# Kernel tuning notes

Measured on AMD Instinct MI355X. Metric: run time of the kernel, lower is better.

The kernel has to match this reference:

```python
import jax, jax.numpy as jnp
import numpy as np
from math import sqrt

KEY_DIM = 128
VALUE_DIM = 128
SUMMARY_DIM = 128
QUESTION_NUM = 10000
CONCEPT_NUM = 64
B = 128
S = 128


def setup_inputs() -> dict:
    key = jax.random.key(0)
    ks = jax.random.split(key, 24)
    stdev = 1.0 / sqrt(CONCEPT_NUM + KEY_DIM)

    def lin_w(k, out_f, in_f):
        bound = 1.0 / sqrt(in_f)
        return jax.random.uniform(k, (out_f, in_f), jnp.float32, -bound, bound)

    def lin_b(k, out_f, in_f):
        bound = 1.0 / sqrt(in_f)
        return jax.random.uniform(k, (out_f,), jnp.float32, -bound, bound)

    q_emb = jax.random.normal(ks[0], (QUESTION_NUM + 1, KEY_DIM), jnp.float32)
    q_emb = q_emb.at[0].set(0.0)  # padding_idx = 0
    i_emb = jax.random.normal(ks[1], (2 * QUESTION_NUM + 1, VALUE_DIM), jnp.float32)
    i_emb = i_emb.at[0].set(0.0)

    inp = {
        "right_input": jax.random.randint(ks[2], (B, S), 0, 2 * QUESTION_NUM + 1),
        "wrong_input": jax.random.randint(ks[3], (B, S), 0, 2 * QUESTION_NUM + 1),
        "target_id": jax.random.randint(ks[4], (B,), 0, QUESTION_NUM + 1),
        "q_emb": q_emb,
        "i_emb": i_emb,
        "key_W": lin_w(ks[5], CONCEPT_NUM, KEY_DIM),  # no bias
        "erase_W": lin_w(ks[6], VALUE_DIM, VALUE_DIM),
        "erase_b": lin_b(ks[7], VALUE_DIM, VALUE_DIM),
        "add_W": lin_w(ks[8], VALUE_DIM, VALUE_DIM),
        "add_b": lin_b(ks[9], VALUE_DIM, VALUE_DIM),
        "rsum_W": lin_w(ks[10], SUMMARY_DIM, VALUE_DIM + KEY_DIM),
        "rsum_b": lin_b(ks[11], SUMMARY_DIM, VALUE_DIM + KEY_DIM),
        "wsum_W": lin_w(ks[12], SUMMARY_DIM, VALUE_DIM + KEY_DIM),
        "wsum_b": lin_b(ks[13], SUMMARY_DIM, VALUE_DIM + KEY_DIM),
        "succ_W": lin_w(ks[14], 1, SUMMARY_DIM),
        "succ_b": lin_b(ks[15], 1, SUMMARY_DIM),
        "fail_W": lin_w(ks[16], 1, SUMMARY_DIM),
        "fail_b": lin_b(ks[17], 1, SUMMARY_DIM),
        "diff_W": lin_w(ks[18], 1, KEY_DIM),
        "diff_b": lin_b(ks[19], 1, KEY_DIM),
        "right_mem_init": jax.random.uniform(ks[20], (VALUE_DIM, CONCEPT_NUM), jnp.float32, -stdev, stdev),
        "wrong_mem_init": jax.random.uniform(ks[21], (VALUE_DIM, CONCEPT_NUM), jnp.float32, -stdev, stdev),
    }
    return inp


def reference(right_input, wrong_input, target_id, q_emb, i_emb, key_W,
              erase_W, erase_b, add_W, add_b, rsum_W, rsum_b, wsum_W, wsum_b,
              succ_W, succ_b, fail_W, fail_b, diff_W, diff_b,
              right_mem_init, wrong_mem_init):
    Q = (i_emb.shape[0] - 1) // 2
    batch = right_input.shape[0]

    def corr(qid):  # (B,) -> (B, C) correlation weights
        return jax.nn.softmax(q_emb[qid] @ key_W.T, axis=-1)

    def update(mem, inter):
        # mem: (B, V, C); inter: (B,) interaction ids
        vec = i_emb[inter]                                  # (B, V)
        e = jax.nn.sigmoid(vec @ erase_W.T + erase_b)       # (B, V)
        a = jnp.tanh(vec @ add_W.T + add_b)                 # (B, V)
        qid = inter - Q * (inter > Q).astype(inter.dtype)
        w = corr(qid)                                       # (B, C)
        # erase/add are outer products w (x) e, w (x) a -> (B, V, C)
        return mem * (1.0 - e[:, :, None] * w[:, None, :]) + a[:, :, None] * w[:, None, :]

    def step(carry, xs):
        rm, wm = carry
        ri, wi = xs
        return (update(rm, ri), update(wm, wi)), None

    rm0 = jnp.broadcast_to(right_mem_init, (batch,) + right_mem_init.shape)
    wm0 = jnp.broadcast_to(wrong_mem_init, (batch,) + wrong_mem_init.shape)
    (rm, wm), _ = jax.lax.scan(step, (rm0, wm0), (right_input.T, wrong_input.T))

    qv = q_emb[target_id]                                   # (B, K)
    w_t = corr(target_id)                                   # (B, C)
    right_read = jnp.einsum('bvc,bc->bv', rm, w_t)          # (B, V)
    wrong_read = jnp.einsum('bvc,bc->bv', wm, w_t)

    r_sum = jnp.tanh(jnp.concatenate([right_read, qv], axis=-1) @ rsum_W.T + rsum_b)
    w_sum = jnp.tanh(jnp.concatenate([wrong_read, qv], axis=-1) @ wsum_W.T + wsum_b)

    success_level = jnp.tanh(r_sum @ succ_W.T + succ_b)     # (B, 1)
    failure_level = jnp.tanh(w_sum @ fail_W.T + fail_b)     # (B, 1)
    difficulty_level = jnp.tanh(qv @ diff_W.T + diff_b)     # (B, 1)

    success_count = jnp.sum(jnp.clip(right_input, 0, 1)).astype(jnp.float32)
    failure_count = jnp.sum(jnp.clip(wrong_input, 0, 1)).astype(jnp.float32)

    out = (success_level * jax.nn.sigmoid(success_count)
           + failure_level * jax.nn.sigmoid(failure_count)
           - difficulty_level * 2.0)
    return out
```

## Files before the change

### kernel.cpp

```cpp
#include <hip/hip_runtime.h>
#include <hip/hip_bf16.h>

#define BB 128
#define SS 128
#define VD 128
#define CN 64
#define KD 128
#define QN 10000

typedef __attribute__((ext_vector_type(8))) short bf16x8;
typedef __attribute__((ext_vector_type(4))) float f32x4;

__device__ __forceinline__ float bflo(unsigned int u) { return __uint_as_float(u << 16); }
__device__ __forceinline__ float bfhi(unsigned int u) { return __uint_as_float(u & 0xffff0000u); }
__device__ __forceinline__ unsigned int cvtpk(float lo, float hi) {
    __hip_bfloat162 h2 = __float22bfloat162_rn(make_float2(lo, hi));
    unsigned int r; __builtin_memcpy(&r, &h2, 4); return r;
}
__device__ __forceinline__ float fast_tanh(float x) {
    float e = __expf(2.0f * x);
    return 1.0f - 2.0f / (e + 1.0f);
}
__device__ __forceinline__ float fast_sig(float x) {
    return 1.0f / (1.0f + __expf(-x));
}

__global__ __launch_bounds__(256) void k_wcnt(
    const float* __restrict__ erase_W, const float* __restrict__ add_W,
    const float* __restrict__ key_W, unsigned short* __restrict__ Bfrag,
    const int* __restrict__ ri, const int* __restrict__ wi, float* __restrict__ sig)
{
    const int t = threadIdx.x;
    if (blockIdx.x < 20) {
        const int bid = blockIdx.x * 4 + (t >> 6);
        const int l = t & 63;
        const int n = (bid >> 2) * 16 + (l & 15);
        const int k0 = (bid & 3) * 32 + (l >> 4) * 8;
        const float* src;
        if (n < 128)      src = erase_W + (size_t)n * KD + k0;
        else if (n < 256) src = add_W + (size_t)(n - 128) * KD + k0;
        else              src = key_W + (size_t)(n - 256) * KD + k0;
        float4 fa = ((const float4*)src)[0];
        float4 fb = ((const float4*)src)[1];
        uint4 o = make_uint4(cvtpk(fa.x, fa.y), cvtpk(fa.z, fa.w), cvtpk(fb.x, fb.y), cvtpk(fb.z, fb.w));
        *(uint4*)(Bfrag + ((size_t)bid * 64 + l) * 8) = o;
    } else {
        __shared__ int sr_s[4], sw_s[4];
        const int4* r4 = (const int4*)ri;
        const int4* w4 = (const int4*)wi;
        int sr = 0, sw = 0;
        #pragma unroll 4
        for (int p = 0; p < 16; ++p) {
            int4 a = r4[p * 256 + t];
            int4 b = w4[p * 256 + t];
            sr += (a.x >= 1) + (a.y >= 1) + (a.z >= 1) + (a.w >= 1);
            sw += (b.x >= 1) + (b.y >= 1) + (b.z >= 1) + (b.w >= 1);
        }
        for (int off = 1; off < 64; off <<= 1) { sr += __shfl_xor(sr, off); sw += __shfl_xor(sw, off); }
        int wid = t >> 6;
        if ((t & 63) == 0) { sr_s[wid] = sr; sw_s[wid] = sw; }
        __syncthreads();
        if (t == 0) {
            int SR = sr_s[0]+sr_s[1]+sr_s[2]+sr_s[3];
            int SW = sw_s[0]+sw_s[1]+sw_s[2]+sw_s[3];
            sig[0] = 1.0f / (1.0f + __expf(-(float)SR));
            sig[1] = 1.0f / (1.0f + __expf(-(float)SW));
        }
    }
}

__global__ __launch_bounds__(1024, 4) void k_chain(
    const int* __restrict__ ri, const int* __restrict__ wi, const int* __restrict__ tgt,
    const float* __restrict__ q_emb, const float* __restrict__ i_emb,
    const float* __restrict__ key_W,
    const float* __restrict__ erase_b, const float* __restrict__ add_b,
    const unsigned short* __restrict__ Bfrag,
    const float* __restrict__ rmem0, const float* __restrict__ wmem0,
    float* __restrict__ readbuf)
{
    __shared__ __align__(16) unsigned int lds_ea[SS * VD];
    __shared__ __align__(16) char xab[32 * 1024];
    __shared__ __align__(16) float logits[SS * 68];
    __shared__ __align__(16) unsigned short lds_w[SS * CN];
    __shared__ float q_t[KD];
    __shared__ float logit_t[CN];
    __shared__ float wt_lds[CN];
    __shared__ int qid_s[SS], ir_s[SS];
    __shared__ float psum[8 * 64];

    const int t = threadIdx.x;
    const int lane = t & 63;
    const int w = t >> 6;
    const int chain = blockIdx.x;
    const int m = chain >> 7;
    const int b = chain & 127;

    if (t < SS) {
        int inter = (m == 0 ? ri : wi)[b * SS + t];
        ir_s[t] = inter;
        qid_s[t] = (inter > QN) ? inter - QN : inter;
        q_t[t] = q_emb[(size_t)tgt[b] * KD + t];
    }
    __syncthreads();

    {
        const int r = t >> 3, o = t & 7;
        const float* src = q_emb + (size_t)qid_s[r] * KD + o * 16;
        float4 f0 = ((const float4*)src)[0];
        float4 f1 = ((const float4*)src)[1];
        float4 f2 = ((const float4*)src)[2];
        float4 f3 = ((const float4*)src)[3];
        const int bb = r * 256 + o * 32;
        const int sw = (r & 7) << 4;
        *(uint4*)(xab + (bb ^ sw))        = make_uint4(cvtpk(f0.x,f0.y), cvtpk(f0.z,f0.w), cvtpk(f1.x,f1.y), cvtpk(f1.z,f1.w));
        *(uint4*)(xab + ((bb + 16) ^ sw)) = make_uint4(cvtpk(f2.x,f2.y), cvtpk(f2.z,f2.w), cvtpk(f3.x,f3.y), cvtpk(f3.z,f3.w));
        if (t < 512) {
            const int c = t >> 3, oct = t & 7;
            const float* kw = key_W + (size_t)c * KD + oct * 16;
            float s = 0.f;
            #pragma unroll
            for (int i = 0; i < 16; ++i) s = fmaf(kw[i], q_t[oct * 16 + i], s);
            s += __shfl_xor(s, 1); s += __shfl_xor(s, 2); s += __shfl_xor(s, 4);
            if (oct == 0) logit_t[c] = s;
        }
    }
    __syncthreads();

    const int rowl = lane & 15;
    const int kb16 = (lane >> 4) * 16;
    const int rb4 = (lane >> 4) * 4;
    const int rt = w & 7;

    {
        if (w == 0) {
            float x = logit_t[lane];
            float mx = x;
            #pragma unroll
            for (int off = 1; off < 64; off <<= 1) mx = fmaxf(mx, __shfl_xor(mx, off));
            float e = __expf(x - mx);
            float ssum = e;
            #pragma unroll
            for (int off = 1; off < 64; off <<= 1) ssum += __shfl_xor(ssum, off);
            wt_lds[lane] = e / ssum;
        }
        bf16x8 afQ[4];
        const int row = rt * 16 + rowl;
        #pragma unroll
        for (int kt = 0; kt < 4; ++kt)
            afQ[kt] = *(const bf16x8*)(xab + ((row * 256 + kt * 64 + kb16) ^ ((row & 7) << 4)));
        const int nt0 = (w >> 3) * 2;
        #pragma unroll
        for (int ni = 0; ni < 2; ++ni) {
            const int nt = nt0 + ni;
            f32x4 acc = {0.f,0.f,0.f,0.f};
            #pragma unroll
            for (int kt = 0; kt < 4; ++kt) {
                bf16x8 bf = *(const bf16x8*)(Bfrag + ((size_t)((16 + nt) * 4 + kt) * 64 + lane) * 8);
                acc = __builtin_amdgcn_mfma_f32_16x16x32_bf16(afQ[kt], bf, acc, 0, 0, 0);
            }
            #pragma unroll
            for (int rr = 0; rr < 4; ++rr)
                logits[(rt * 16 + rb4 + rr) * 68 + nt * 16 + rowl] = acc[rr];
        }
    }
    __syncthreads();

    {
        const int rr = t >> 3, q = t & 7;
        const float* L = logits + rr * 68 + q * 8;
        float4 va = ((const float4*)L)[0];
        float4 vb = ((const float4*)L)[1];
        float mx = fmaxf(fmaxf(fmaxf(va.x, va.y), fmaxf(va.z, va.w)),
                         fmaxf(fmaxf(vb.x, vb.y), fmaxf(vb.z, vb.w)));
        mx = fmaxf(mx, __shfl_xor(mx, 1));
        mx = fmaxf(mx, __shfl_xor(mx, 2));
        mx = fmaxf(mx, __shfl_xor(mx, 4));
        float e0 = __expf(va.x - mx), e1 = __expf(va.y - mx), e2 = __expf(va.z - mx), e3 = __expf(va.w - mx);
        float e4 = __expf(vb.x - mx), e5 = __expf(vb.y - mx), e6 = __expf(vb.z - mx), e7 = __expf(vb.w - mx);
        float s = e0 + e1 + e2 + e3 + e4 + e5 + e6 + e7;
        s += __shfl_xor(s, 1); s += __shfl_xor(s, 2); s += __shfl_xor(s, 4);
        float inv = 1.0f / s;
        uint4 o = make_uint4(cvtpk(e0*inv, e1*inv), cvtpk(e2*inv, e3*inv),
                             cvtpk(e4*inv, e5*inv), cvtpk(e6*inv, e7*inv));
        *(uint4*)(lds_w + rr * CN + q * 8) = o;

        const float* src = i_emb + (size_t)ir_s[rr] * KD + q * 16;
        float4 f0 = ((const float4*)src)[0];
        float4 f1 = ((const float4*)src)[1];
        float4 f2 = ((const float4*)src)[2];
        float4 f3 = ((const float4*)src)[3];
        const int bb = rr * 256 + q * 32;
        const int sw = (rr & 7) << 4;
        *(uint4*)(xab + (bb ^ sw))        = make_uint4(cvtpk(f0.x,f0.y), cvtpk(f0.z,f0.w), cvtpk(f1.x,f1.y), cvtpk(f1.z,f1.w));
        *(uint4*)(xab + ((bb + 16) ^ sw)) = make_uint4(cvtpk(f2.x,f2.y), cvtpk(f2.z,f2.w), cvtpk(f3.x,f3.y), cvtpk(f3.z,f3.w));
    }
    __syncthreads();

    {
        bf16x8 afI[4];
        const int row = rt * 16 + rowl;
        #pragma unroll
        for (int kt = 0; kt < 4; ++kt)
            afI[kt] = *(const bf16x8*)(xab + ((row * 256 + kt * 64 + kb16) ^ ((row & 7) << 4)));
        const int ci0 = (w >> 3) * 4;
        #pragma unroll
        for (int ii = 0; ii < 4; ++ii) {
            const int ci = ci0 + ii;
            f32x4 ae = {0.f,0.f,0.f,0.f}, aa = {0.f,0.f,0.f,0.f};
            #pragma unroll
            for (int kt = 0; kt < 4; ++kt) {
                bf16x8 be = *(const bf16x8*)(Bfrag + ((size_t)(ci * 4 + kt) * 64 + lane) * 8);
                bf16x8 ba = *(const bf16x8*)(Bfrag + ((size_t)((8 + ci) * 4 + kt) * 64 + lane) * 8);
                ae = __builtin_amdgcn_mfma_f32_16x16x32_bf16(afI[kt], be, ae, 0, 0, 0);
                aa = __builtin_amdgcn_mfma_f32_16x16x32_bf16(afI[kt], ba, aa, 0, 0, 0);
            }
            const int cc = ci * 16 + rowl;
            const float bvE = erase_b[cc];
            const float bvA = add_b[cc];
            #pragma unroll
            for (int rr = 0; rr < 4; ++rr) {
                float e = fast_sig(ae[rr] + bvE);
                float a = fast_tanh(aa[rr] + bvA);
                lds_ea[(rt * 16 + rb4 + rr) * VD + cc] = cvtpk(e, a);
            }
        }
    }

    const int w2 = w & 7;
    const int vhalf = w2 & 1;
    const int cq = w2 >> 1;
    const int vg = lane >> 2;
    const int cg = lane & 3;
    const int v0 = vhalf * 64 + vg * 4;
    const int c0 = cq * 16 + cg * 4;

    float mm[4][4];
    if (t < 512) {
        const float* minit = (m == 0) ? rmem0 : wmem0;
        #pragma unroll
        for (int j = 0; j < 4; ++j) {
            float4 mi = *(const float4*)(minit + (v0 + j) * CN + c0);
            mm[j][0] = mi.x; mm[j][1] = mi.y; mm[j][2] = mi.z; mm[j][3] = mi.w;
        }
    }
    __syncthreads();

    if (t < 512) {
        for (int so = 0; so < 16; ++so) {
            const unsigned int* eap = lds_ea + (so * 8) * VD + v0;
            const unsigned short* wp = lds_w + (so * 8) * CN + c0;
            #pragma unroll
            for (int kk = 0; kk < 8; ++kk) {
                uint4 ea = *(const uint4*)(eap + kk * VD);
                uint2 wu = *(const uint2*)(wp + kk * CN);
                float e[4] = { bflo(ea.x), bflo(ea.y), bflo(ea.z), bflo(ea.w) };
                float a[4] = { bfhi(ea.x), bfhi(ea.y), bfhi(ea.z), bfhi(ea.w) };
                float wv[4] = { bflo(wu.x), bfhi(wu.x), bflo(wu.y), bfhi(wu.y) };
                #pragma unroll
                for (int j = 0; j < 4; ++j) {
                    #pragma unroll
                    for (int k = 0; k < 4; ++k) {
                        float g = fmaf(-e[j], mm[j][k], a[j]);
                        mm[j][k] = fmaf(wv[k], g, mm[j][k]);
                    }
                }
            }
        }

        float4 wt = *(const float4*)(wt_lds + c0);
        float p[4];
        #pragma unroll
        for (int j = 0; j < 4; ++j) {
            float x = mm[j][0] * wt.x;
            x = fmaf(mm[j][1], wt.y, x);
            x = fmaf(mm[j][2], wt.z, x);
            x = fmaf(mm[j][3], wt.w, x);
            p[j] = x;
        }
        #pragma unroll
        for (int j = 0; j < 4; ++j) {
            p[j] += __shfl_xor(p[j], 1);
            p[j] += __shfl_xor(p[j], 2);
        }
        if (cg == 0) {
            #pragma unroll
            for (int j = 0; j < 4; ++j) psum[w2 * 64 + vg * 4 + j] = p[j];
        }
    }
    __syncthreads();
    if (t < 128) {
        const int vh = t >> 6, vl = t & 63;
        float s = psum[(0 * 2 + vh) * 64 + vl] + psum[(1 * 2 + vh) * 64 + vl]
                + psum[(2 * 2 + vh) * 64 + vl] + psum[(3 * 2 + vh) * 64 + vl];
        readbuf[(size_t)chain * VD + t] = s;
    }
}

__global__ __launch_bounds__(256) void k_head(
    const float* __restrict__ readbuf, const int* __restrict__ tgt,
    const float* __restrict__ q_emb,
    const float* __restrict__ rsum_W, const float* __restrict__ rsum_b,
    const float* __restrict__ wsum_W, const float* __restrict__ wsum_b,
    const float* __restrict__ succ_W, const float* __restrict__ succ_b,
    const float* __restrict__ fail_W, const float* __restrict__ fail_b,
    const float* __restrict__ diff_W, const float* __restrict__ diff_b,
    const float* __restrict__ sig, float* __restrict__ out)
{
    __shared__ float xr[256], xw[256];
    __shared__ float part[2][128];
    __shared__ float red_s[6];
    const int t = threadIdx.x;
    const int j = t & 127;
    const int h = t >> 7;
    const int b = blockIdx.x;
    if (h == 0) {
        int tid_ = tgt[b];
        float qv = q_emb[(size_t)tid_ * KD + j];
        xr[j]       = readbuf[(size_t)b * VD + j];
        xr[128 + j] = qv;
        xw[j]       = readbuf[(size_t)(BB + b) * VD + j];
        xw[128 + j] = qv;
    }
    __syncthreads();

    float rs = (h == 0) ? rsum_b[j] : 0.0f;
    float wv = (h == 0) ? wsum_b[j] : 0.0f;
    const float* rw = rsum_W + (size_t)j * 256 + h * 128;
    const float* ww = wsum_W + (size_t)j * 256 + h * 128;
    const float* xrp = xr + h * 128;
    const float* xwp = xw + h * 128;
    #pragma unroll 4
    for (int k = 0; k < 128; ++k) {
        rs = fmaf(rw[k], xrp[k], rs);
        wv = fmaf(ww[k], xwp[k], wv);
    }
    if (h == 1) { part[0][j] = rs; part[1][j] = wv; }
    __syncthreads();
    if (h == 0) {
        rs += part[0][j];
        wv += part[1][j];
        float r_sum = fast_tanh(rs), w_sum = fast_tanh(wv);
        float qv = xr[128 + j];
        float ps = r_sum * succ_W[j];
        float pf = w_sum * fail_W[j];
        float pd = qv    * diff_W[j];
        for (int off = 1; off < 64; off <<= 1) {
            ps += __shfl_xor(ps, off);
            pf += __shfl_xor(pf, off);
            pd += __shfl_xor(pd, off);
        }
        int wid = j >> 6;
        if ((j & 63) == 0) { red_s[wid*3+0] = ps; red_s[wid*3+1] = pf; red_s[wid*3+2] = pd; }
    }
    __syncthreads();
    if (t == 0) {
        float Ps = red_s[0] + red_s[3];
        float Pf = red_s[1] + red_s[4];
        float Pd = red_s[2] + red_s[5];
        float succ = fast_tanh(Ps + succ_b[0]);
        float fail = fast_tanh(Pf + fail_b[0]);
        float diff = fast_tanh(Pd + diff_b[0]);
        out[b] = succ * sig[0] + fail * sig[1] - 2.0f * diff;
    }
}

extern "C" void kernel_launch(void* const* d_in, const int* in_sizes, int n_in,
                              void* d_out, int out_size, void* d_ws, size_t ws_size,
                              hipStream_t stream) {
    const int*   ri      = (const int*)d_in[0];
    const int*   wi      = (const int*)d_in[1];
    const int*   tgt     = (const int*)d_in[2];
    const float* q_emb   = (const float*)d_in[3];
    const float* i_emb   = (const float*)d_in[4];
    const float* key_W   = (const float*)d_in[5];
    const float* erase_W = (const float*)d_in[6];
    const float* erase_b = (const float*)d_in[7];
    const float* add_W   = (const float*)d_in[8];
    const float* add_b   = (const float*)d_in[9];
    const float* rsum_W  = (const float*)d_in[10];
    const float* rsum_b  = (const float*)d_in[11];
    const float* wsum_W  = (const float*)d_in[12];
    const float* wsum_b  = (const float*)d_in[13];
    const float* succ_W  = (const float*)d_in[14];
    const float* succ_b  = (const float*)d_in[15];
    const float* fail_W  = (const float*)d_in[16];
    const float* fail_b  = (const float*)d_in[17];
    const float* diff_W  = (const float*)d_in[18];
    const float* diff_b  = (const float*)d_in[19];
    const float* rmem0   = (const float*)d_in[20];
    const float* wmem0   = (const float*)d_in[21];

    char* ws = (char*)d_ws;
    float*          readbuf = (float*)(ws + 0);
    unsigned short* Bfrag   = (unsigned short*)(ws + 131072);
    float*          sig     = (float*)(ws + 212992);
    float*          out     = (float*)d_out;

    hipLaunchKernelGGL(k_wcnt, dim3(21), dim3(256), 0, stream,
        erase_W, add_W, key_W, Bfrag, ri, wi, sig);
    hipLaunchKernelGGL(k_chain, dim3(256), dim3(1024), 0, stream,
        ri, wi, tgt, q_emb, i_emb, key_W, erase_b, add_b, Bfrag,
        rmem0, wmem0, readbuf);
    hipLaunchKernelGGL(k_head, dim3(128), dim3(256), 0, stream,
        readbuf, tgt, q_emb, rsum_W, rsum_b, wsum_W, wsum_b,
        succ_W, succ_b, fail_W, fail_b, diff_W, diff_b, sig, out);
}
```

Before: 50.16 us.

## Overlap second-half embedding/MFMA prologue with memory scan via warp specialization

Splits the block's 16 waves into two groups. The first half of the sequence's gathers, logits and erase/add gates are computed by all waves. Then waves 8-15 begin the sequential memory-update scan on those first 64 steps while waves 0-7 gather, project and gate the remaining 64 steps in stages. This hides the prologue latency behind the serial scan, at the cost of more barriers and fewer waves doing each MFMA phase.

```diff
diff --git a/kernel.cpp b/kernel.cpp
--- a/kernel.cpp
+++ b/kernel.cpp
@@ -95,6 +95,19 @@
     const int m = chain >> 7;
     const int b = chain & 127;
 
+    const int rowl = lane & 15;
+    const int kb16 = (lane >> 4) * 16;
+    const int rb4 = (lane >> 4) * 4;
+
+    const int w2 = w & 7;
+    const int vhalf = w2 & 1;
+    const int cq = w2 >> 1;
+    const int vg = lane >> 2;
+    const int cg = lane & 3;
+    const int v0 = vhalf * 64 + vg * 4;
+    const int c0 = cq * 16 + cg * 4;
+    float mm[4][4];
+
     if (t < SS) {
         int inter = (m == 0 ? ri : wi)[b * SS + t];
         ir_s[t] = inter;
@@ -103,7 +116,7 @@
     }
     __syncthreads();
 
-    {
+    if (t < 512) {
         const int r = t >> 3, o = t & 7;
         const float* src = q_emb + (size_t)qid_s[r] * KD + o * 16;
         float4 f0 = ((const float4*)src)[0];
@@ -114,22 +127,16 @@
         const int sw = (r & 7) << 4;
         *(uint4*)(xab + (bb ^ sw))        = make_uint4(cvtpk(f0.x,f0.y), cvtpk(f0.z,f0.w), cvtpk(f1.x,f1.y), cvtpk(f1.z,f1.w));
         *(uint4*)(xab + ((bb + 16) ^ sw)) = make_uint4(cvtpk(f2.x,f2.y), cvtpk(f2.z,f2.w), cvtpk(f3.x,f3.y), cvtpk(f3.z,f3.w));
-        if (t < 512) {
-            const int c = t >> 3, oct = t & 7;
-            const float* kw = key_W + (size_t)c * KD + oct * 16;
-            float s = 0.f;
-            #pragma unroll
-            for (int i = 0; i < 16; ++i) s = fmaf(kw[i], q_t[oct * 16 + i], s);
-            s += __shfl_xor(s, 1); s += __shfl_xor(s, 2); s += __shfl_xor(s, 4);
-            if (oct == 0) logit_t[c] = s;
-        }
-    }
-    __syncthreads();
-
-    const int rowl = lane & 15;
-    const int kb16 = (lane >> 4) * 16;
-    const int rb4 = (lane >> 4) * 4;
-    const int rt = w & 7;
+    } else {
+        const int c = (t >> 3) & 63, oct = t & 7;
+        const float* kw = key_W + (size_t)c * KD + oct * 16;
+        float s = 0.f;
+        #pragma unroll
+        for (int i = 0; i < 16; ++i) s = fmaf(kw[i], q_t[oct * 16 + i], s);
+        s += __shfl_xor(s, 1); s += __shfl_xor(s, 2); s += __shfl_xor(s, 4);
+        if (oct == 0) logit_t[c] = s;
+    }
+    __syncthreads();
 
     {
         if (w == 0) {
@@ -143,29 +150,26 @@
             for (int off = 1; off < 64; off <<= 1) ssum += __shfl_xor(ssum, off);
             wt_lds[lane] = e / ssum;
         }
+        const int rt = w & 3;
+        const int nt = w >> 2;
         bf16x8 afQ[4];
         const int row = rt * 16 + rowl;
         #pragma unroll
         for (int kt = 0; kt < 4; ++kt)
             afQ[kt] = *(const bf16x8*)(xab + ((row * 256 + kt * 64 + kb16) ^ ((row & 7) << 4)));
-        const int nt0 = (w >> 3) * 2;
-        #pragma unroll
-        for (int ni = 0; ni < 2; ++ni) {
-            const int nt = nt0 + ni;
-            f32x4 acc = {0.f,0.f,0.f,0.f};
-            #pragma unroll
-            for (int kt = 0; kt < 4; ++kt) {
-                bf16x8 bf = *(const bf16x8*)(Bfrag + ((size_t)((16 + nt) * 4 + kt) * 64 + lane) * 8);
-                acc = __builtin_amdgcn_mfma_f32_16x16x32_bf16(afQ[kt], bf, acc, 0, 0, 0);
-            }
-            #pragma unroll
-            for (int rr = 0; rr < 4; ++rr)
-                logits[(rt * 16 + rb4 + rr) * 68 + nt * 16 + rowl] = acc[rr];
-        }
-    }
-    __syncthreads();
-
-    {
+        f32x4 acc = {0.f,0.f,0.f,0.f};
+        #pragma unroll
+        for (int kt = 0; kt < 4; ++kt) {
+            bf16x8 bf = *(const bf16x8*)(Bfrag + ((size_t)((16 + nt) * 4 + kt) * 64 + lane) * 8);
+            acc = __builtin_amdgcn_mfma_f32_16x16x32_bf16(afQ[kt], bf, acc, 0, 0, 0);
+        }
+        #pragma unroll
+        for (int rr = 0; rr < 4; ++rr)
+            logits[(rt * 16 + rb4 + rr) * 68 + nt * 16 + rowl] = acc[rr];
+    }
+    __syncthreads();
+
+    if (t < 512) {
         const int rr = t >> 3, q = t & 7;
         const float* L = logits + rr * 68 + q * 8;
         float4 va = ((const float4*)L)[0];
@@ -183,6 +187,143 @@
         uint4 o = make_uint4(cvtpk(e0*inv, e1*inv), cvtpk(e2*inv, e3*inv),
                              cvtpk(e4*inv, e5*inv), cvtpk(e6*inv, e7*inv));
         *(uint4*)(lds_w + rr * CN + q * 8) = o;
+    } else {
+        const int r = (t >> 3) - 64, o = t & 7;
+        const float* src = i_emb + (size_t)ir_s[r] * KD + o * 16;
+        float4 f0 = ((const float4*)src)[0];
+        float4 f1 = ((const float4*)src)[1];
+        float4 f2 = ((const float4*)src)[2];
+        float4 f3 = ((const float4*)src)[3];
+        const int bb = r * 256 + o * 32;
+        const int sw = (r & 7) << 4;
+        *(uint4*)(xab + (bb ^ sw))        = make_uint4(cvtpk(f0.x,f0.y), cvtpk(f0.z,f0.w), cvtpk(f1.x,f1.y), cvtpk(f1.z,f1.w));
+        *(uint4*)(xab + ((bb + 16) ^ sw)) = make_uint4(cvtpk(f2.x,f2.y), cvtpk(f2.z,f2.w), cvtpk(f3.x,f3.y), cvtpk(f3.z,f3.w));
+    }
+    __syncthreads();
+
+    {
+        const int rt = w & 3;
+        bf16x8 afI[4];
+        const int row = rt * 16 + rowl;
+        #pragma unroll
+        for (int kt = 0; kt < 4; ++kt)
+            afI[kt] = *(const bf16x8*)(xab + ((row * 256 + kt * 64 + kb16) ^ ((row & 7) << 4)));
+        const int ci0 = (w >> 2) * 2;
+        #pragma unroll
+        for (int ii = 0; ii < 2; ++ii) {
+            const int ci = ci0 + ii;
+            f32x4 ae = {0.f,0.f,0.f,0.f}, aa = {0.f,0.f,0.f,0.f};
+            #pragma unroll
+            for (int kt = 0; kt < 4; ++kt) {
+                bf16x8 be = *(const bf16x8*)(Bfrag + ((size_t)(ci * 4 + kt) * 64 + lane) * 8);
+                bf16x8 ba = *(const bf16x8*)(Bfrag + ((size_t)((8 + ci) * 4 + kt) * 64 + lane) * 8);
+                ae = __builtin_amdgcn_mfma_f32_16x16x32_bf16(afI[kt], be, ae, 0, 0, 0);
+                aa = __builtin_amdgcn_mfma_f32_16x16x32_bf16(afI[kt], ba, aa, 0, 0, 0);
+            }
+            const int cc = ci * 16 + rowl;
+            const float bvE = erase_b[cc];
+            const float bvA = add_b[cc];
+            #pragma unroll
+            for (int rr = 0; rr < 4; ++rr) {
+                float e = fast_sig(ae[rr] + bvE);
+                float a = fast_tanh(aa[rr] + bvA);
+                lds_ea[(rt * 16 + rb4 + rr) * VD + cc] = cvtpk(e, a);
+            }
+        }
+    }
+
+    if (w >= 8) {
+        const float* minit = (m == 0) ? rmem0 : wmem0;
+        #pragma unroll
+        for (int j = 0; j < 4; ++j) {
+            float4 mi = *(const float4*)(minit + (v0 + j) * CN + c0);
+            mm[j][0] = mi.x; mm[j][1] = mi.y; mm[j][2] = mi.z; mm[j][3] = mi.w;
+        }
+    }
+    __syncthreads();
+
+#define SCAN_CHUNK(S0, NSO)                                                     \
+    for (int so = (S0); so < (S0) + (NSO); ++so) {                              \
+        const unsigned int* eap = lds_ea + (so * 8) * VD + v0;                  \
+        const unsigned short* wp = lds_w + (so * 8) * CN + c0;                  \
+        _Pragma("unroll")                                                       \
+        for (int kk = 0; kk < 8; ++kk) {                                        \
+            uint4 ea = *(const uint4*)(eap + kk * VD);                          \
+            uint2 wu = *(const uint2*)(wp + kk * CN);                           \
+            float e[4] = { bflo(ea.x), bflo(ea.y), bflo(ea.z), bflo(ea.w) };    \
+            float a[4] = { bfhi(ea.x), bfhi(ea.y), bfhi(ea.z), bfhi(ea.w) };    \
+            float wv[4] = { bflo(wu.x), bfhi(wu.x), bflo(wu.y), bfhi(wu.y) };   \
+            _Pragma("unroll")                                                   \
+            for (int j = 0; j < 4; ++j) {                                       \
+                _Pragma("unroll")                                               \
+                for (int k = 0; k < 4; ++k) {                                   \
+                    float g = fmaf(-e[j], mm[j][k], a[j]);                      \
+                    mm[j][k] = fmaf(wv[k], g, mm[j][k]);                        \
+                }                                                               \
+            }                                                                   \
+        }                                                                       \
+    }
+
+    if (w < 8) {
+        const int r = 64 + (t >> 3), o = t & 7;
+        const float* src = q_emb + (size_t)qid_s[r] * KD + o * 16;
+        float4 f0 = ((const float4*)src)[0];
+        float4 f1 = ((const float4*)src)[1];
+        float4 f2 = ((const float4*)src)[2];
+        float4 f3 = ((const float4*)src)[3];
+        const int bb = r * 256 + o * 32;
+        const int sw = (r & 7) << 4;
+        *(uint4*)(xab + (bb ^ sw))        = make_uint4(cvtpk(f0.x,f0.y), cvtpk(f0.z,f0.w), cvtpk(f1.x,f1.y), cvtpk(f1.z,f1.w));
+        *(uint4*)(xab + ((bb + 16) ^ sw)) = make_uint4(cvtpk(f2.x,f2.y), cvtpk(f2.z,f2.w), cvtpk(f3.x,f3.y), cvtpk(f3.z,f3.w));
+    } else {
+        SCAN_CHUNK(0, 2)
+    }
+    __syncthreads();
+
+    if (w < 8) {
+        const int rt = 4 + (w & 3);
+        bf16x8 afQ[4];
+        const int row = rt * 16 + rowl;
+        #pragma unroll
+        for (int kt = 0; kt < 4; ++kt)
+            afQ[kt] = *(const bf16x8*)(xab + ((row * 256 + kt * 64 + kb16) ^ ((row & 7) << 4)));
+        const int nt0 = (w >> 2) * 2;
+        #pragma unroll
+        for (int ni = 0; ni < 2; ++ni) {
+            const int nt = nt0 + ni;
+            f32x4 acc = {0.f,0.f,0.f,0.f};
+            #pragma unroll
+            for (int kt = 0; kt < 4; ++kt) {
+                bf16x8 bf = *(const bf16x8*)(Bfrag + ((size_t)((16 + nt) * 4 + kt) * 64 + lane) * 8);
+                acc = __builtin_amdgcn_mfma_f32_16x16x32_bf16(afQ[kt], bf, acc, 0, 0, 0);
+            }
+            #pragma unroll
+            for (int rr = 0; rr < 4; ++rr)
+                logits[(rt * 16 + rb4 + rr) * 68 + nt * 16 + rowl] = acc[rr];
+        }
+    } else {
+        SCAN_CHUNK(2, 2)
+    }
+    __syncthreads();
+
+    if (w < 8) {
+        const int rr = 64 + (t >> 3), q = t & 7;
+        const float* L = logits + rr * 68 + q * 8;
+        float4 va = ((const float4*)L)[0];
+        float4 vb = ((const float4*)L)[1];
+        float mx = fmaxf(fmaxf(fmaxf(va.x, va.y), fmaxf(va.z, va.w)),
+                         fmaxf(fmaxf(vb.x, vb.y), fmaxf(vb.z, vb.w)));
+        mx = fmaxf(mx, __shfl_xor(mx, 1));
+        mx = fmaxf(mx, __shfl_xor(mx, 2));
+        mx = fmaxf(mx, __shfl_xor(mx, 4));
+        float e0 = __expf(va.x - mx), e1 = __expf(va.y - mx), e2 = __expf(va.z - mx), e3 = __expf(va.w - mx);
+        float e4 = __expf(vb.x - mx), e5 = __expf(vb.y - mx), e6 = __expf(vb.z - mx), e7 = __expf(vb.w - mx);
+        float s = e0 + e1 + e2 + e3 + e4 + e5 + e6 + e7;
+        s += __shfl_xor(s, 1); s += __shfl_xor(s, 2); s += __shfl_xor(s, 4);
+        float inv = 1.0f / s;
+        uint4 o = make_uint4(cvtpk(e0*inv, e1*inv), cvtpk(e2*inv, e3*inv),
+                             cvtpk(e4*inv, e5*inv), cvtpk(e6*inv, e7*inv));
+        *(uint4*)(lds_w + rr * CN + q * 8) = o;
 
         const float* src = i_emb + (size_t)ir_s[rr] * KD + q * 16;
         float4 f0 = ((const float4*)src)[0];
@@ -193,16 +334,19 @@
         const int sw = (rr & 7) << 4;
         *(uint4*)(xab + (bb ^ sw))        = make_uint4(cvtpk(f0.x,f0.y), cvtpk(f0.z,f0.w), cvtpk(f1.x,f1.y), cvtpk(f1.z,f1.w));
         *(uint4*)(xab + ((bb + 16) ^ sw)) = make_uint4(cvtpk(f2.x,f2.y), cvtpk(f2.z,f2.w), cvtpk(f3.x,f3.y), cvtpk(f3.z,f3.w));
-    }
-    __syncthreads();
-
-    {
+    } else {
+        SCAN_CHUNK(4, 2)
+    }
+    __syncthreads();
+
+    if (w < 8) {
+        const int rt = 4 + (w & 3);
         bf16x8 afI[4];
         const int row = rt * 16 + rowl;
         #pragma unroll
         for (int kt = 0; kt < 4; ++kt)
             afI[kt] = *(const bf16x8*)(xab + ((row * 256 + kt * 64 + kb16) ^ ((row & 7) << 4)));
-        const int ci0 = (w >> 3) * 4;
+        const int ci0 = (w >> 2) * 4;
         #pragma unroll
         for (int ii = 0; ii < 4; ++ii) {
             const int ci = ci0 + ii;
@@ -224,48 +368,13 @@
                 lds_ea[(rt * 16 + rb4 + rr) * VD + cc] = cvtpk(e, a);
             }
         }
-    }
-
-    const int w2 = w & 7;
-    const int vhalf = w2 & 1;
-    const int cq = w2 >> 1;
-    const int vg = lane >> 2;
-    const int cg = lane & 3;
-    const int v0 = vhalf * 64 + vg * 4;
-    const int c0 = cq * 16 + cg * 4;
-
-    float mm[4][4];
-    if (t < 512) {
-        const float* minit = (m == 0) ? rmem0 : wmem0;
-        #pragma unroll
-        for (int j = 0; j < 4; ++j) {
-            float4 mi = *(const float4*)(minit + (v0 + j) * CN + c0);
-            mm[j][0] = mi.x; mm[j][1] = mi.y; mm[j][2] = mi.z; mm[j][3] = mi.w;
-        }
-    }
-    __syncthreads();
-
-    if (t < 512) {
-        for (int so = 0; so < 16; ++so) {
-            const unsigned int* eap = lds_ea + (so * 8) * VD + v0;
-            const unsigned short* wp = lds_w + (so * 8) * CN + c0;
-            #pragma unroll
-            for (int kk = 0; kk < 8; ++kk) {
-                uint4 ea = *(const uint4*)(eap + kk * VD);
-                uint2 wu = *(const uint2*)(wp + kk * CN);
-                float e[4] = { bflo(ea.x), bflo(ea.y), bflo(ea.z), bflo(ea.w) };
-                float a[4] = { bfhi(ea.x), bfhi(ea.y), bfhi(ea.z), bfhi(ea.w) };
-                float wv[4] = { bflo(wu.x), bfhi(wu.x), bflo(wu.y), bfhi(wu.y) };
-                #pragma unroll
-                for (int j = 0; j < 4; ++j) {
-                    #pragma unroll
-                    for (int k = 0; k < 4; ++k) {
-                        float g = fmaf(-e[j], mm[j][k], a[j]);
-                        mm[j][k] = fmaf(wv[k], g, mm[j][k]);
-                    }
-                }
-            }
-        }
+    } else {
+        SCAN_CHUNK(6, 2)
+    }
+    __syncthreads();
+
+    if (w >= 8) {
+        SCAN_CHUNK(8, 8)
 
         float4 wt = *(const float4*)(wt_lds + c0);
         float p[4];
@@ -294,6 +403,7 @@
                 + psum[(2 * 2 + vh) * 64 + vl] + psum[(3 * 2 + vh) * 64 + vl];
         readbuf[(size_t)chain * VD + t] = s;
     }
+#undef SCAN_CHUNK
 }
 
 __global__ __launch_bounds__(256) void k_head(
```

New measurement: 50.61 us. About the same (+0.9%).

## Build MFMA fragments straight from global memory and fuse softmax into key GEMM

Applied to the files above, without the earlier changes.

Removes the LDS staging buffers for question and interaction embeddings and the logits scratch. MFMA A-fragments are now converted to bf16 directly from global rows in registers. The key-attention softmax runs on the MFMA accumulators using lane shuffles, and warps are specialised so the interaction fragment load, target weights and memory init overlap with the key GEMM. The recurrent update loop moves to waves 8-15. This cuts LDS traffic, LDS footprint and one or two barriers, at the cost of redundant global loads of i_emb rows and more register pressure.

```diff
diff --git a/kernel.cpp b/kernel.cpp
--- a/kernel.cpp
+++ b/kernel.cpp
@@ -17,12 +17,29 @@
     __hip_bfloat162 h2 = __float22bfloat162_rn(make_float2(lo, hi));
     unsigned int r; __builtin_memcpy(&r, &h2, 4); return r;
 }
+__device__ __forceinline__ bf16x8 mk8(unsigned int a, unsigned int b,
+                                      unsigned int c, unsigned int d) {
+    union { uint4 u; bf16x8 v; } x;
+    x.u = make_uint4(a, b, c, d);
+    return x.v;
+}
 __device__ __forceinline__ float fast_tanh(float x) {
     float e = __expf(2.0f * x);
     return 1.0f - 2.0f / (e + 1.0f);
 }
 __device__ __forceinline__ float fast_sig(float x) {
     return 1.0f / (1.0f + __expf(-x));
+}
+
+__device__ __forceinline__ void build_frag(const float* __restrict__ rowp, int kb8,
+                                           bf16x8 af[4]) {
+    #pragma unroll
+    for (int kt = 0; kt < 4; ++kt) {
+        const float* s8 = rowp + kt * 32 + kb8;
+        float4 a = *(const float4*)s8;
+        float4 c = *(const float4*)(s8 + 4);
+        af[kt] = mk8(cvtpk(a.x, a.y), cvtpk(a.z, a.w), cvtpk(c.x, c.y), cvtpk(c.z, c.w));
+    }
 }
 
 __global__ __launch_bounds__(256) void k_wcnt(
@@ -79,11 +96,7 @@
     float* __restrict__ readbuf)
 {
     __shared__ __align__(16) unsigned int lds_ea[SS * VD];
-    __shared__ __align__(16) char xab[32 * 1024];
-    __shared__ __align__(16) float logits[SS * 68];
     __shared__ __align__(16) unsigned short lds_w[SS * CN];
-    __shared__ float q_t[KD];
-    __shared__ float logit_t[CN];
     __shared__ float wt_lds[CN];
     __shared__ int qid_s[SS], ir_s[SS];
     __shared__ float psum[8 * 64];
@@ -95,136 +108,11 @@
     const int m = chain >> 7;
     const int b = chain & 127;
 
-    if (t < SS) {
-        int inter = (m == 0 ? ri : wi)[b * SS + t];
-        ir_s[t] = inter;
-        qid_s[t] = (inter > QN) ? inter - QN : inter;
-        q_t[t] = q_emb[(size_t)tgt[b] * KD + t];
-    }
-    __syncthreads();
-
-    {
-        const int r = t >> 3, o = t & 7;
-        const float* src = q_emb + (size_t)qid_s[r] * KD + o * 16;
-        float4 f0 = ((const float4*)src)[0];
-        float4 f1 = ((const float4*)src)[1];
-        float4 f2 = ((const float4*)src)[2];
-        float4 f3 = ((const float4*)src)[3];
-        const int bb = r * 256 + o * 32;
-        const int sw = (r & 7) << 4;
-        *(uint4*)(xab + (bb ^ sw))        = make_uint4(cvtpk(f0.x,f0.y), cvtpk(f0.z,f0.w), cvtpk(f1.x,f1.y), cvtpk(f1.z,f1.w));
-        *(uint4*)(xab + ((bb + 16) ^ sw)) = make_uint4(cvtpk(f2.x,f2.y), cvtpk(f2.z,f2.w), cvtpk(f3.x,f3.y), cvtpk(f3.z,f3.w));
-        if (t < 512) {
-            const int c = t >> 3, oct = t & 7;
-            const float* kw = key_W + (size_t)c * KD + oct * 16;
-            float s = 0.f;
-            #pragma unroll
-            for (int i = 0; i < 16; ++i) s = fmaf(kw[i], q_t[oct * 16 + i], s);
-            s += __shfl_xor(s, 1); s += __shfl_xor(s, 2); s += __shfl_xor(s, 4);
-            if (oct == 0) logit_t[c] = s;
-        }
-    }
-    __syncthreads();
-
     const int rowl = lane & 15;
-    const int kb16 = (lane >> 4) * 16;
-    const int rb4 = (lane >> 4) * 4;
+    const int g4 = lane >> 4;
+    const int kb8 = g4 * 8;
+    const int rb4 = g4 * 4;
     const int rt = w & 7;
-
-    {
-        if (w == 0) {
-            float x = logit_t[lane];
-            float mx = x;
-            #pragma unroll
-            for (int off = 1; off < 64; off <<= 1) mx = fmaxf(mx, __shfl_xor(mx, off));
-            float e = __expf(x - mx);
-            float ssum = e;
-            #pragma unroll
-            for (int off = 1; off < 64; off <<= 1) ssum += __shfl_xor(ssum, off);
-            wt_lds[lane] = e / ssum;
-        }
-        bf16x8 afQ[4];
-        const int row = rt * 16 + rowl;
-        #pragma unroll
-        for (int kt = 0; kt < 4; ++kt)
-            afQ[kt] = *(const bf16x8*)(xab + ((row * 256 + kt * 64 + kb16) ^ ((row & 7) << 4)));
-        const int nt0 = (w >> 3) * 2;
-        #pragma unroll
-        for (int ni = 0; ni < 2; ++ni) {
-            const int nt = nt0 + ni;
-            f32x4 acc = {0.f,0.f,0.f,0.f};
-            #pragma unroll
-            for (int kt = 0; kt < 4; ++kt) {
-                bf16x8 bf = *(const bf16x8*)(Bfrag + ((size_t)((16 + nt) * 4 + kt) * 64 + lane) * 8);
-                acc = __builtin_amdgcn_mfma_f32_16x16x32_bf16(afQ[kt], bf, acc, 0, 0, 0);
-            }
-            #pragma unroll
-            for (int rr = 0; rr < 4; ++rr)
-                logits[(rt * 16 + rb4 + rr) * 68 + nt * 16 + rowl] = acc[rr];
-        }
-    }
-    __syncthreads();
-
-    {
-        const int rr = t >> 3, q = t & 7;
-        const float* L = logits + rr * 68 + q * 8;
-        float4 va = ((const float4*)L)[0];
-        float4 vb = ((const float4*)L)[1];
-        float mx = fmaxf(fmaxf(fmaxf(va.x, va.y), fmaxf(va.z, va.w)),
-                         fmaxf(fmaxf(vb.x, vb.y), fmaxf(vb.z, vb.w)));
-        mx = fmaxf(mx, __shfl_xor(mx, 1));
-        mx = fmaxf(mx, __shfl_xor(mx, 2));
-        mx = fmaxf(mx, __shfl_xor(mx, 4));
-        float e0 = __expf(va.x - mx), e1 = __expf(va.y - mx), e2 = __expf(va.z - mx), e3 = __expf(va.w - mx);
-        float e4 = __expf(vb.x - mx), e5 = __expf(vb.y - mx), e6 = __expf(vb.z - mx), e7 = __expf(vb.w - mx);
-        float s = e0 + e1 + e2 + e3 + e4 + e5 + e6 + e7;
-        s += __shfl_xor(s, 1); s += __shfl_xor(s, 2); s += __shfl_xor(s, 4);
-        float inv = 1.0f / s;
-        uint4 o = make_uint4(cvtpk(e0*inv, e1*inv), cvtpk(e2*inv, e3*inv),
-                             cvtpk(e4*inv, e5*inv), cvtpk(e6*inv, e7*inv));
-        *(uint4*)(lds_w + rr * CN + q * 8) = o;
-
-        const float* src = i_emb + (size_t)ir_s[rr] * KD + q * 16;
-        float4 f0 = ((const float4*)src)[0];
-        float4 f1 = ((const float4*)src)[1];
-        float4 f2 = ((const float4*)src)[2];
-        float4 f3 = ((const float4*)src)[3];
-        const int bb = rr * 256 + q * 32;
-        const int sw = (rr & 7) << 4;
-        *(uint4*)(xab + (bb ^ sw))        = make_uint4(cvtpk(f0.x,f0.y), cvtpk(f0.z,f0.w), cvtpk(f1.x,f1.y), cvtpk(f1.z,f1.w));
-        *(uint4*)(xab + ((bb + 16) ^ sw)) = make_uint4(cvtpk(f2.x,f2.y), cvtpk(f2.z,f2.w), cvtpk(f3.x,f3.y), cvtpk(f3.z,f3.w));
-    }
-    __syncthreads();
-
-    {
-        bf16x8 afI[4];
-        const int row = rt * 16 + rowl;
-        #pragma unroll
-        for (int kt = 0; kt < 4; ++kt)
-            afI[kt] = *(const bf16x8*)(xab + ((row * 256 + kt * 64 + kb16) ^ ((row & 7) << 4)));
-        const int ci0 = (w >> 3) * 4;
-        #pragma unroll
-        for (int ii = 0; ii < 4; ++ii) {
-            const int ci = ci0 + ii;
-            f32x4 ae = {0.f,0.f,0.f,0.f}, aa = {0.f,0.f,0.f,0.f};
-            #pragma unroll
-            for (int kt = 0; kt < 4; ++kt) {
-                bf16x8 be = *(const bf16x8*)(Bfrag + ((size_t)(ci * 4 + kt) * 64 + lane) * 8);
-                bf16x8 ba = *(const bf16x8*)(Bfrag + ((size_t)((8 + ci) * 4 + kt) * 64 + lane) * 8);
-                ae = __builtin_amdgcn_mfma_f32_16x16x32_bf16(afI[kt], be, ae, 0, 0, 0);
-                aa = __builtin_amdgcn_mfma_f32_16x16x32_bf16(afI[kt], ba, aa, 0, 0, 0);
-            }
-            const int cc = ci * 16 + rowl;
-            const float bvE = erase_b[cc];
-            const float bvA = add_b[cc];
-            #pragma unroll
-            for (int rr = 0; rr < 4; ++rr) {
-                float e = fast_sig(ae[rr] + bvE);
-                float a = fast_tanh(aa[rr] + bvA);
-                lds_ea[(rt * 16 + rb4 + rr) * VD + cc] = cvtpk(e, a);
-            }
-        }
-    }
 
     const int w2 = w & 7;
     const int vhalf = w2 & 1;
@@ -233,9 +121,88 @@
     const int cg = lane & 3;
     const int v0 = vhalf * 64 + vg * 4;
     const int c0 = cq * 16 + cg * 4;
-
     float mm[4][4];
-    if (t < 512) {
+
+    if (t < SS) {
+        int inter = (m == 0 ? ri : wi)[b * SS + t];
+        ir_s[t] = inter;
+        qid_s[t] = (inter > QN) ? inter - QN : inter;
+    }
+    __syncthreads();
+
+    bf16x8 afI[4];
+    const int rowg = rt * 16 + rowl;
+
+    if (w < 8) {
+        bf16x8 afQ[4];
+        build_frag(q_emb + (size_t)qid_s[rowg] * KD, kb8, afQ);
+        f32x4 accK[4];
+        #pragma unroll
+        for (int nt = 0; nt < 4; ++nt) {
+            f32x4 acc = {0.f, 0.f, 0.f, 0.f};
+            #pragma unroll
+            for (int kt = 0; kt < 4; ++kt) {
+                bf16x8 bf = *(const bf16x8*)(Bfrag + ((size_t)((16 + nt) * 4 + kt) * 64 + lane) * 8);
+                acc = __builtin_amdgcn_mfma_f32_16x16x32_bf16(afQ[kt], bf, acc, 0, 0, 0);
+            }
+            accK[nt] = acc;
+        }
+        unsigned int* w32 = (unsigned int*)lds_w;
+        #pragma unroll
+        for (int rr = 0; rr < 4; ++rr) {
+            float mx = fmaxf(fmaxf(accK[0][rr], accK[1][rr]), fmaxf(accK[2][rr], accK[3][rr]));
+            mx = fmaxf(mx, __shfl_xor(mx, 1));
+            mx = fmaxf(mx, __shfl_xor(mx, 2));
+            mx = fmaxf(mx, __shfl_xor(mx, 4));
+            mx = fmaxf(mx, __shfl_xor(mx, 8));
+            float e0 = __expf(accK[0][rr] - mx);
+            float e1 = __expf(accK[1][rr] - mx);
+            float e2 = __expf(accK[2][rr] - mx);
+            float e3 = __expf(accK[3][rr] - mx);
+            float s = e0 + e1 + e2 + e3;
+            s += __shfl_xor(s, 1);
+            s += __shfl_xor(s, 2);
+            s += __shfl_xor(s, 4);
+            s += __shfl_xor(s, 8);
+            float inv = 1.0f / s;
+            e0 *= inv; e1 *= inv; e2 *= inv; e3 *= inv;
+            float n0 = __shfl_xor(e0, 1);
+            float n1 = __shfl_xor(e1, 1);
+            float n2 = __shfl_xor(e2, 1);
+            float n3 = __shfl_xor(e3, 1);
+            if (!(lane & 1)) {
+                const int rowst = (rt * 16 + rb4 + rr) * 32;
+                const int ch = rowl >> 1;
+                w32[rowst + 0 * 8 + ch] = cvtpk(e0, n0);
+                w32[rowst + 1 * 8 + ch] = cvtpk(e1, n1);
+                w32[rowst + 2 * 8 + ch] = cvtpk(e2, n2);
+                w32[rowst + 3 * 8 + ch] = cvtpk(e3, n3);
+            }
+        }
+    } else {
+        build_frag(i_emb + (size_t)ir_s[rowg] * KD, kb8, afI);
+        if (w == 8) {
+            const float* kw = key_W + (size_t)lane * KD;
+            const float* qt = q_emb + (size_t)tgt[b] * KD;
+            float acc = 0.f;
+            #pragma unroll 8
+            for (int k4 = 0; k4 < 32; ++k4) {
+                float4 kv = *(const float4*)(kw + k4 * 4);
+                float4 qv = *(const float4*)(qt + k4 * 4);
+                acc = fmaf(kv.x, qv.x, acc);
+                acc = fmaf(kv.y, qv.y, acc);
+                acc = fmaf(kv.z, qv.z, acc);
+                acc = fmaf(kv.w, qv.w, acc);
+            }
+            float mx = acc;
+            #pragma unroll
+            for (int off = 1; off < 64; off <<= 1) mx = fmaxf(mx, __shfl_xor(mx, off));
+            float e = __expf(acc - mx);
+            float s = e;
+            #pragma unroll
+            for (int off = 1; off < 64; off <<= 1) s += __shfl_xor(s, off);
+            wt_lds[lane] = e / s;
+        }
         const float* minit = (m == 0) ? rmem0 : wmem0;
         #pragma unroll
         for (int j = 0; j < 4; ++j) {
@@ -245,7 +212,35 @@
     }
     __syncthreads();
 
-    if (t < 512) {
+    {
+        if (w < 8)
+            build_frag(i_emb + (size_t)ir_s[rowg] * KD, kb8, afI);
+        const int ci0 = (w >> 3) * 4;
+        #pragma unroll
+        for (int ii = 0; ii < 4; ++ii) {
+            const int ci = ci0 + ii;
+            f32x4 ae = {0.f,0.f,0.f,0.f}, aa = {0.f,0.f,0.f,0.f};
+            #pragma unroll
+            for (int kt = 0; kt < 4; ++kt) {
+                bf16x8 be = *(const bf16x8*)(Bfrag + ((size_t)(ci * 4 + kt) * 64 + lane) * 8);
+                bf16x8 ba = *(const bf16x8*)(Bfrag + ((size_t)((8 + ci) * 4 + kt) * 64 + lane) * 8);
+                ae = __builtin_amdgcn_mfma_f32_16x16x32_bf16(afI[kt], be, ae, 0, 0, 0);
+                aa = __builtin_amdgcn_mfma_f32_16x16x32_bf16(afI[kt], ba, aa, 0, 0, 0);
+            }
+            const int cc = ci * 16 + rowl;
+            const float bvE = erase_b[cc];
+            const float bvA = add_b[cc];
+            #pragma unroll
+            for (int rr = 0; rr < 4; ++rr) {
+                float e = fast_sig(ae[rr] + bvE);
+                float a = fast_tanh(aa[rr] + bvA);
+                lds_ea[(rt * 16 + rb4 + rr) * VD + cc] = cvtpk(e, a);
+            }
+        }
+    }
+    __syncthreads();
+
+    if (w >= 8) {
         for (int so = 0; so < 16; ++so) {
             const unsigned int* eap = lds_ea + (so * 8) * VD + v0;
             const unsigned short* wp = lds_w + (so * 8) * CN + c0;
```

New measurement: 53.33 us. +6.3%, slower.
